# Optimization experiments

Measured on AMD Instinct MI355X. Metric: run time of the kernel, lower is better.

The kernel has to match this reference:

```python
import jax, jax.numpy as jnp
import numpy as np

N = 50000          # nodes
E = 1000000        # edges (k=20 avg degree)
SD = 32            # scalar_dim = hidden_dim//2
VD = 32            # vector_dim = hidden_dim//2
L = 3              # num_layers
SPIN = 2           # spin_symmetry
IN_DIM = 2 * SD + VD + 3   # message MLP input dim = 99
OUT_DIM = SD + VD          # 64


def setup_inputs() -> dict:
    key = jax.random.key(0)
    ks = jax.random.split(key, 12)
    pos = jax.random.uniform(ks[0], (N, 2), dtype=jnp.float32)
    redshift = jax.random.uniform(ks[1], (N, 1), dtype=jnp.float32)
    input_shapes = jax.random.normal(ks[2], (N, 2), dtype=jnp.float32)
    edge_index = jax.random.randint(ks[3], (2, E), 0, N, dtype=jnp.int64)
    # encoder params
    enc_s_w = jax.random.normal(ks[4], (SD, 1), dtype=jnp.float32) * 0.5
    enc_s_b = jax.random.normal(ks[5], (SD,), dtype=jnp.float32) * 0.1
    enc_v_w = jax.random.normal(ks[6], (VD, 2), dtype=jnp.float32) * 0.5
    # per-layer message MLP params, stacked over layers
    W1 = jax.random.normal(ks[7], (L, OUT_DIM, IN_DIM), dtype=jnp.float32) * (1.0 / np.sqrt(IN_DIM))
    b1 = jax.random.normal(ks[8], (L, OUT_DIM), dtype=jnp.float32) * 0.1
    W2 = jax.random.normal(ks[9], (L, OUT_DIM, OUT_DIM), dtype=jnp.float32) * (1.0 / np.sqrt(OUT_DIM))
    b2 = jax.random.normal(ks[10], (L, OUT_DIM), dtype=jnp.float32) * 0.1
    return {"pos": pos, "redshift": redshift, "input_shapes": input_shapes,
            "edge_index": edge_index, "enc_s_w": enc_s_w, "enc_s_b": enc_s_b,
            "enc_v_w": enc_v_w, "W1": W1, "b1": b1, "W2": W2, "b2": b2}


def _frame_layer(h_s, h_v, pos, orientation, src, dst, W1, b1, W2, b2):
    # per-edge geometric features
    dpos = pos[src] - pos[dst]                                   # [E,2]
    dist = jnp.sqrt(jnp.sum(dpos * dpos, axis=1)) + 1e-6          # [E]
    phi_global = jnp.arctan2(dpos[:, 1], dpos[:, 0])              # [E]
    alpha_i = orientation[dst, 0]                                 # [E]
    delta_phi = phi_global - alpha_i
    geo = jnp.stack([dist, jnp.cos(SPIN * delta_phi), jnp.sin(SPIN * delta_phi)], axis=-1)  # [E,3]
    # rotate source vector features into destination local frame
    beta_j = orientation[src, 0]
    rot = (beta_j - alpha_i) * SPIN
    c, s = jnp.cos(rot)[:, None], jnp.sin(rot)[:, None]           # [E,1]
    v_j = h_v[src].reshape(-1, VD // 2, 2)                        # [E,nv,2]
    vx = v_j[..., 0] * c - v_j[..., 1] * s
    vy = v_j[..., 0] * s + v_j[..., 1] * c
    v_rot = jnp.stack([vx, vy], axis=-1).reshape(-1, VD)          # [E,VD]
    # message MLP
    msg_in = jnp.concatenate([h_s[src], h_s[dst], v_rot, geo], axis=-1)  # [E,IN_DIM]
    hid = jax.nn.silu(msg_in @ W1.T + b1)
    raw = hid @ W2.T + b2                                         # [E,OUT_DIM]
    msg_s, msg_v = raw[:, :SD], raw[:, SD:]
    # scatter-add to destination nodes
    out_s = jax.ops.segment_sum(msg_s, dst, num_segments=h_s.shape[0])
    out_v = jax.ops.segment_sum(msg_v, dst, num_segments=h_v.shape[0])
    return h_s + out_s, h_v + out_v


def reference(pos, redshift, input_shapes, edge_index, enc_s_w, enc_s_b, enc_v_w, W1, b1, W2, b2):
    src, dst = edge_index[0], edge_index[1]
    h_s = jax.nn.relu(redshift @ enc_s_w.T + enc_s_b)             # [N,SD]
    h_v = input_shapes @ enc_v_w.T                                # [N,VD]
    orientation = jnp.zeros((pos.shape[0], 1), dtype=pos.dtype)
    for l in range(L):
        h_s, h_v = _frame_layer(h_s, h_v, pos, orientation, src, dst,
                                W1[l], b1[l], W2[l], b2[l])
    return h_s, h_v
```

## Files before the change

### kernel.cpp

```cpp
#include <hip/hip_runtime.h>
#include <hip/hip_bf16.h>

#define WPB 4
#define TILE 16

typedef unsigned short ushort_t;
typedef unsigned int uint_t;

__device__ __forceinline__ float silu_f(float x) {
  return x * __builtin_amdgcn_rcpf(1.0f + __expf(-x));
}
__device__ __forceinline__ int rfl(int x) { return __builtin_amdgcn_readfirstlane(x); }
__device__ __forceinline__ float readlane_f(float v, int l) {
  return __int_as_float(__builtin_amdgcn_readlane(__float_as_int(v), l));
}
__device__ __forceinline__ ushort_t f2bf(float f) {
  uint_t u = __float_as_uint(f);
  u += 0x7FFFu + ((u >> 16) & 1u);
  return (ushort_t)(u >> 16);
}
__device__ __forceinline__ float bf2f(ushort_t b) {
  return __uint_as_float(((uint_t)b) << 16);
}

__global__ void zero_kernel(int* __restrict__ p, int n) {
  int i = blockIdx.x * blockDim.x + threadIdx.x;
  if (i < n) p[i] = 0;
}

__global__ void deg_kernel(const int* __restrict__ ei, int* __restrict__ deg, int E_) {
  int e = blockIdx.x * blockDim.x + threadIdx.x;
  if (e < E_) atomicAdd(&deg[ei[E_ + e]], 1);
}

__global__ __launch_bounds__(1024) void scanA_kernel(const int* __restrict__ deg,
                                                     int* __restrict__ rowptr,
                                                     int* __restrict__ bsum, int n) {
  __shared__ int wsum[16];
  int t = threadIdx.x, lane = t & 63, wid = t >> 6;
  int i = blockIdx.x * 1024 + t;
  int v = (i < n) ? deg[i] : 0;
  int x = v;
#pragma unroll
  for (int off = 1; off < 64; off <<= 1) {
    int y = __shfl_up(x, off);
    if (lane >= off) x += y;
  }
  if (lane == 63) wsum[wid] = x;
  __syncthreads();
  if (t == 0) {
    int run = 0;
#pragma unroll
    for (int w = 0; w < 16; ++w) { int s = wsum[w]; wsum[w] = run; run += s; }
  }
  __syncthreads();
  int inc = x + wsum[wid];
  if (i < n) rowptr[i + 1] = inc;
  if (t == 1023) bsum[blockIdx.x] = inc;
}

__global__ __launch_bounds__(1024) void scanB_kernel(int* __restrict__ bsum, int nb) {
  __shared__ int wsum[16];
  int t = threadIdx.x, lane = t & 63, wid = t >> 6;
  int v = (t < nb) ? bsum[t] : 0;
  int x = v;
#pragma unroll
  for (int off = 1; off < 64; off <<= 1) {
    int y = __shfl_up(x, off);
    if (lane >= off) x += y;
  }
  if (lane == 63) wsum[wid] = x;
  __syncthreads();
  if (t == 0) {
    int run = 0;
#pragma unroll
    for (int w = 0; w < 16; ++w) { int s = wsum[w]; wsum[w] = run; run += s; }
  }
  __syncthreads();
  if (t < nb) bsum[t] = x - v + wsum[wid];
}

__global__ void scanC_kernel(int* __restrict__ rowptr, const int* __restrict__ bsum, int n) {
  int i = blockIdx.x * blockDim.x + threadIdx.x;
  if (i == 0) rowptr[0] = 0;
  if (i < n) rowptr[i + 1] += bsum[i >> 10];
}

__global__ void scatter_kernel(const int* __restrict__ ei, const float* __restrict__ pos,
                               const int* __restrict__ rowptr, int* __restrict__ cursor,
                               float4* __restrict__ edata,
                               int E_, int padE, int N_) {
  int e = blockIdx.x * blockDim.x + threadIdx.x;
  if (e >= padE) return;
  if (e >= E_) {
    edata[e] = make_float4(0.f, 0.f, __int_as_float(0), __int_as_float(N_));
    return;
  }
  int s = ei[e];
  int d = ei[E_ + e];
  int idx = rowptr[d] + atomicAdd(&cursor[d], 1);
  float dx = pos[s * 2 + 0] - pos[d * 2 + 0];
  float dy = pos[s * 2 + 1] - pos[d * 2 + 1];
  float r2 = fmaf(dx, dx, dy * dy);
  float dist = sqrtf(r2) + 1e-6f;
  float c2 = 1.0f, s2 = 0.0f;
  if (r2 > 0.0f) {
    float inv = 1.0f / r2;
    c2 = (dx * dx - dy * dy) * inv;
    s2 = 2.0f * dx * dy * inv;
  }
  uint_t pk = ((uint_t)f2bf(s2) << 16) | (uint_t)f2bf(c2);
  edata[idx] = make_float4(dist, __uint_as_float(pk),
                           __int_as_float(s), __int_as_float(d));
}

__global__ __launch_bounds__(256) void encpsd_kernel(
    const float* __restrict__ redshift, const float* __restrict__ shapes,
    const float* __restrict__ enc_s_w, const float* __restrict__ enc_s_b,
    const float* __restrict__ enc_v_w,
    float* __restrict__ hout, const float* __restrict__ W1l,
    const float* __restrict__ b1l,
    ushort_t* __restrict__ PSh, ushort_t* __restrict__ PDBh,
    float* __restrict__ H, int N_) {
  __shared__ float wsh[99 * 64];
  __shared__ float esw[32], esb[32], evw[64];
  __shared__ __align__(16) float hsh[TILE][64];
  int t = threadIdx.x;
  for (int i = t; i < 99 * 64; i += 256) wsh[i] = W1l[i];
  if (t < 32) { esw[t] = enc_s_w[t]; esb[t] = enc_s_b[t]; }
  else if (t < 96) { evw[t - 32] = enc_v_w[t - 32]; }
  __syncthreads();
  int lane = t & 63, wib = t >> 6;
  float ws_[32], wd_[32], wv_[32];
#pragma unroll
  for (int k = 0; k < 32; ++k) {
    ws_[k] = wsh[lane * 99 + k];
    wd_[k] = wsh[lane * 99 + 32 + k];
    wv_[k] = wsh[lane * 99 + 64 + k];
  }
  float bb1 = b1l[lane];
  const int nTiles = (N_ + TILE - 1) / TILE;
  float* hvbase = hout + (size_t)N_ * 32;
  int tt = t & 127;
  int sn = tt >> 3;
  int sc = tt & 7;
  for (int tile = blockIdx.x; tile < nTiles; tile += gridDim.x) {
    int base = tile * TILE;
    {
      int n = base + sn;
      float4 v = make_float4(0.f, 0.f, 0.f, 0.f);
      if (n < N_) {
        if (t < 128) {
          float r = redshift[n];
#pragma unroll
          for (int jj = 0; jj < 4; ++jj) {
            int j = sc * 4 + jj;
            (&v.x)[jj] = fmaxf(fmaf(r, esw[j], esb[j]), 0.0f);
          }
          *reinterpret_cast<float4*>(hout + (size_t)n * 32 + sc * 4) = v;
        } else {
          float x0 = shapes[n * 2 + 0];
          float x1 = shapes[n * 2 + 1];
#pragma unroll
          for (int jj = 0; jj < 4; ++jj) {
            int j = sc * 4 + jj;
            (&v.x)[jj] = fmaf(x0, evw[j * 2 + 0], x1 * evw[j * 2 + 1]);
          }
          *reinterpret_cast<float4*>(hvbase + (size_t)n * 32 + sc * 4) = v;
        }
      }
      *reinterpret_cast<float4*>(&hsh[sn][(t < 128 ? 0 : 32) + sc * 4]) = v;
    }
    __syncthreads();
#pragma unroll
    for (int q = 0; q < 4; ++q) {
      int r = wib + q * 4;
      int n = base + r;
      if (n < N_) {
        const float4* ha = reinterpret_cast<const float4*>(hsh[r]);
        float ps0 = 0.f, ps1 = 0.f, ps2 = 0.f, ps3 = 0.f, pd0 = 0.f, pd1 = 0.f;
#pragma unroll
        for (int k4 = 0; k4 < 8; ++k4) {
          float4 a = ha[k4];
          float4 v = ha[8 + k4];
          int k = k4 * 4;
          ps0 = fmaf(a.x, ws_[k], ps0);     pd0 = fmaf(a.x, wd_[k], pd0);
          ps1 = fmaf(a.y, ws_[k + 1], ps1); pd1 = fmaf(a.y, wd_[k + 1], pd1);
          ps2 = fmaf(a.z, ws_[k + 2], ps2); pd0 = fmaf(a.z, wd_[k + 2], pd0);
          ps3 = fmaf(a.w, ws_[k + 3], ps3); pd1 = fmaf(a.w, wd_[k + 3], pd1);
          ps0 = fmaf(v.x, wv_[k], ps0);
          ps1 = fmaf(v.y, wv_[k + 1], ps1);
          ps2 = fmaf(v.z, wv_[k + 2], ps2);
          ps3 = fmaf(v.w, wv_[k + 3], ps3);
        }
        PSh[(size_t)n * 64 + lane] = f2bf((ps0 + ps1) + (ps2 + ps3));
        PDBh[(size_t)n * 64 + lane] = f2bf((pd0 + pd1) + bb1);
        H[(size_t)n * 64 + lane] = 0.0f;
      }
    }
    __syncthreads();
  }
}

#define ISSUE(P, G)                                             \
  do {                                                          \
    int t0 = __builtin_amdgcn_readlane(sv, (G) + 0);            \
    int t1 = __builtin_amdgcn_readlane(sv, (G) + 1);            \
    int t2 = __builtin_amdgcn_readlane(sv, (G) + 2);            \
    int t3 = __builtin_amdgcn_readlane(sv, (G) + 3);            \
    int t4 = __builtin_amdgcn_readlane(sv, (G) + 4);            \
    int t5 = __builtin_amdgcn_readlane(sv, (G) + 5);            \
    int t6 = __builtin_amdgcn_readlane(sv, (G) + 6);            \
    int t7 = __builtin_amdgcn_readlane(sv, (G) + 7);            \
    P##0 = PSh[(size_t)t0 * 64 + lane];                         \
    P##1 = PSh[(size_t)t1 * 64 + lane];                         \
    P##2 = PSh[(size_t)t2 * 64 + lane];                         \
    P##3 = PSh[(size_t)t3 * 64 + lane];                         \
    P##4 = PSh[(size_t)t4 * 64 + lane];                         \
    P##5 = PSh[(size_t)t5 * 64 + lane];                         \
    P##6 = PSh[(size_t)t6 * 64 + lane];                         \
    P##7 = PSh[(size_t)t7 * 64 + lane];                         \
  } while (0)

#define FLUSH()                                                          \
  do {                                                                   \
    atomicAdd(H + (size_t)dcur * 64 + lane, acc0 + acc1);                \
    acc0 = acc1 = 0.0f;                                                  \
    dcur = dnext;                                                        \
    pdj = pdj_next;                                                      \
    bmask &= bmask - 1;                                                  \
    bnext = bmask ? (int)__builtin_ctzll(bmask) : 64;                    \
    dnext = (bnext < 64) ? __builtin_amdgcn_readlane(dv, bnext) : dcur;  \
    pdj_next = bf2f(PDBh[(size_t)dnext * 64 + lane]);                    \
  } while (0)

#define EDGE_ONE(PSV, E)                                                     \
  do {                                                                       \
    if ((E) == bnext) FLUSH();                                               \
    float psv = bf2f((ushort_t)(PSV));                                       \
    float di = readlane_f(ed.x, (E));                                        \
    uint_t pk = (uint_t)__builtin_amdgcn_readlane(__float_as_int(ed.y), (E));\
    float c2 = __uint_as_float(pk << 16);                                    \
    float s2 = __uint_as_float(pk & 0xFFFF0000u);                            \
    float pre = fmaf(wg0, di, fmaf(wg1, c2, fmaf(wg2, s2, psv + pdj)));      \
    if ((E) & 1) acc1 += silu_f(pre); else acc0 += silu_f(pre);              \
  } while (0)

#define CONSUME(P, G)                                            \
  do {                                                           \
    EDGE_ONE(P##0, (G) + 0); EDGE_ONE(P##1, (G) + 1);            \
    EDGE_ONE(P##2, (G) + 2); EDGE_ONE(P##3, (G) + 3);            \
    EDGE_ONE(P##4, (G) + 4); EDGE_ONE(P##5, (G) + 5);            \
    EDGE_ONE(P##6, (G) + 6); EDGE_ONE(P##7, (G) + 7);            \
  } while (0)

__global__ __launch_bounds__(256) void edge_kernel(
    const ushort_t* __restrict__ PSh, const ushort_t* __restrict__ PDBh,
    const float4* __restrict__ edata,
    const float* __restrict__ W1l, float* __restrict__ H, int nchunk) {
  int lane = threadIdx.x & 63, wib = threadIdx.x >> 6;
  int chunk = blockIdx.x * WPB + wib;
  if (chunk >= nchunk) return;
  int base = chunk << 6;
  float wg0 = W1l[lane * 99 + 96];
  float wg1 = W1l[lane * 99 + 97];
  float wg2 = W1l[lane * 99 + 98];
  float4 ed = edata[base + lane];
  int sv = __float_as_int(ed.z);
  int dv = __float_as_int(ed.w);
  int dprev = __shfl_up(dv, 1);
  unsigned long long bmask = __ballot(dv != dprev) & ~1ull;
  int dcur = rfl(dv);
  float pdj = bf2f(PDBh[(size_t)dcur * 64 + lane]);
  int bnext = bmask ? (int)__builtin_ctzll(bmask) : 64;
  int dnext = (bnext < 64) ? __builtin_amdgcn_readlane(dv, bnext) : dcur;
  float pdj_next = bf2f(PDBh[(size_t)dnext * 64 + lane]);
  float acc0 = 0.0f, acc1 = 0.0f;
  uint_t pA0, pA1, pA2, pA3, pA4, pA5, pA6, pA7;
  uint_t pB0, pB1, pB2, pB3, pB4, pB5, pB6, pB7;
  uint_t pC0, pC1, pC2, pC3, pC4, pC5, pC6, pC7;
  uint_t pD0, pD1, pD2, pD3, pD4, pD5, pD6, pD7;
  ISSUE(pA, 0);
  ISSUE(pB, 8);
  ISSUE(pC, 16);
  ISSUE(pD, 24);
  CONSUME(pA, 0);
  ISSUE(pA, 32);
  CONSUME(pB, 8);
  ISSUE(pB, 40);
  CONSUME(pC, 16);
  ISSUE(pC, 48);
  CONSUME(pD, 24);
  ISSUE(pD, 56);
  CONSUME(pA, 32);
  CONSUME(pB, 40);
  CONSUME(pC, 48);
  CONSUME(pD, 56);
  atomicAdd(H + (size_t)dcur * 64 + lane, acc0 + acc1);
}

__global__ __launch_bounds__(256) void updproj_kernel(
    float* __restrict__ hout, float* __restrict__ H,
    const int* __restrict__ deg,
    const float* __restrict__ W2l, const float* __restrict__ b2l,
    const float* __restrict__ W1n, const float* __restrict__ b1n,
    ushort_t* __restrict__ PSh, ushort_t* __restrict__ PDBh, int N_) {
  __shared__ float w2sh[64 * 65];
  __shared__ float wsh[99 * 64];
  __shared__ __align__(16) float Hsh[TILE][64];
  int t = threadIdx.x;
  for (int i = t; i < 64 * 64; i += 256) w2sh[(i >> 6) * 65 + (i & 63)] = W2l[i];
  for (int i = t; i < 99 * 64; i += 256) wsh[i] = W1n[i];
  __syncthreads();
  int lane = t & 63, wib = t >> 6;
  float w2[64];
#pragma unroll
  for (int k = 0; k < 64; ++k) w2[k] = w2sh[lane * 65 + k];
  float ws_[32], wd_[32], wv_[32];
#pragma unroll
  for (int k = 0; k < 32; ++k) {
    ws_[k] = wsh[lane * 99 + k];
    wd_[k] = wsh[lane * 99 + 32 + k];
    wv_[k] = wsh[lane * 99 + 64 + k];
  }
  float bb2 = b2l[lane];
  float bb1 = b1n[lane];
  const int nTiles = (N_ + TILE - 1) / TILE;
  size_t plane = (size_t)(lane >> 5) * ((size_t)N_ * 32);
  int sn = t >> 4;
  int sc = t & 15;
  for (int tile = blockIdx.x; tile < nTiles; tile += gridDim.x) {
    int base = tile * TILE;
    {
      int n = base + sn;
      float4 v = (n < N_) ? *reinterpret_cast<const float4*>(H + (size_t)n * 64 + sc * 4)
                          : make_float4(0.f, 0.f, 0.f, 0.f);
      *reinterpret_cast<float4*>(&Hsh[sn][sc * 4]) = v;
    }
    __syncthreads();
#pragma unroll
    for (int q = 0; q < 4; ++q) {
      int r = wib + q * 4;
      int n = base + r;
      if (n < N_) {
        const float4* hm = reinterpret_cast<const float4*>(Hsh[r]);
        float o0 = 0.f, o1 = 0.f;
#pragma unroll
        for (int k4 = 0; k4 < 16; k4 += 2) {
          float4 m0 = hm[k4];
          float4 m1 = hm[k4 + 1];
          o0 = fmaf(m0.x, w2[k4 * 4 + 0], o0);
          o0 = fmaf(m0.y, w2[k4 * 4 + 1], o0);
          o0 = fmaf(m0.z, w2[k4 * 4 + 2], o0);
          o0 = fmaf(m0.w, w2[k4 * 4 + 3], o0);
          o1 = fmaf(m1.x, w2[k4 * 4 + 4], o1);
          o1 = fmaf(m1.y, w2[k4 * 4 + 5], o1);
          o1 = fmaf(m1.z, w2[k4 * 4 + 6], o1);
          o1 = fmaf(m1.w, w2[k4 * 4 + 7], o1);
        }
        float degf = (float)deg[n];
        size_t idx = plane + (size_t)n * 32 + (lane & 31);
        float hnew = hout[idx] + (o0 + o1) + degf * bb2;
        hout[idx] = hnew;
        Hsh[r][lane] = hnew;
        asm volatile("s_waitcnt lgkmcnt(0)" ::: "memory");
        const float4* ha = reinterpret_cast<const float4*>(Hsh[r]);
        float ps0 = 0.f, ps1 = 0.f, ps2 = 0.f, ps3 = 0.f, pd0 = 0.f, pd1 = 0.f;
#pragma unroll
        for (int k4 = 0; k4 < 8; ++k4) {
          float4 a = ha[k4];
          float4 v = ha[8 + k4];
          int k = k4 * 4;
          ps0 = fmaf(a.x, ws_[k], ps0);     pd0 = fmaf(a.x, wd_[k], pd0);
          ps1 = fmaf(a.y, ws_[k + 1], ps1); pd1 = fmaf(a.y, wd_[k + 1], pd1);
          ps2 = fmaf(a.z, ws_[k + 2], ps2); pd0 = fmaf(a.z, wd_[k + 2], pd0);
          ps3 = fmaf(a.w, ws_[k + 3], ps3); pd1 = fmaf(a.w, wd_[k + 3], pd1);
          ps0 = fmaf(v.x, wv_[k], ps0);
          ps1 = fmaf(v.y, wv_[k + 1], ps1);
          ps2 = fmaf(v.z, wv_[k + 2], ps2);
          ps3 = fmaf(v.w, wv_[k + 3], ps3);
        }
        PSh[(size_t)n * 64 + lane] = f2bf((ps0 + ps1) + (ps2 + ps3));
        PDBh[(size_t)n * 64 + lane] = f2bf((pd0 + pd1) + bb1);
        H[(size_t)n * 64 + lane] = 0.0f;
      }
    }
    __syncthreads();
  }
}

__global__ __launch_bounds__(256) void out_kernel(
    float* __restrict__ hout, const float* __restrict__ H,
    const int* __restrict__ deg,
    const float* __restrict__ W2l, const float* __restrict__ b2l, int N_) {
  __shared__ float w2sh[64 * 65];
  __shared__ __align__(16) float Hsh[TILE][64];
  int t = threadIdx.x;
  for (int i = t; i < 64 * 64; i += 256) w2sh[(i >> 6) * 65 + (i & 63)] = W2l[i];
  __syncthreads();
  int lane = t & 63, wib = t >> 6;
  float w2[64];
#pragma unroll
  for (int k = 0; k < 64; ++k) w2[k] = w2sh[lane * 65 + k];
  float bb2 = b2l[lane];
  const int nTiles = (N_ + TILE - 1) / TILE;
  size_t plane = (size_t)(lane >> 5) * ((size_t)N_ * 32);
  int sn = t >> 4;
  int sc = t & 15;
  for (int tile = blockIdx.x; tile < nTiles; tile += gridDim.x) {
    int base = tile * TILE;
    {
      int n = base + sn;
      float4 v = (n < N_) ? *reinterpret_cast<const float4*>(H + (size_t)n * 64 + sc * 4)
                          : make_float4(0.f, 0.f, 0.f, 0.f);
      *reinterpret_cast<float4*>(&Hsh[sn][sc * 4]) = v;
    }
    __syncthreads();
#pragma unroll
    for (int q = 0; q < 4; ++q) {
      int r = wib + q * 4;
      int n = base + r;
      if (n < N_) {
        const float4* hm = reinterpret_cast<const float4*>(Hsh[r]);
        float o0 = 0.f, o1 = 0.f;
#pragma unroll
        for (int k4 = 0; k4 < 16; k4 += 2) {
          float4 m0 = hm[k4];
          float4 m1 = hm[k4 + 1];
          o0 = fmaf(m0.x, w2[k4 * 4 + 0], o0);
          o0 = fmaf(m0.y, w2[k4 * 4 + 1], o0);
          o0 = fmaf(m0.z, w2[k4 * 4 + 2], o0);
          o0 = fmaf(m0.w, w2[k4 * 4 + 3], o0);
          o1 = fmaf(m1.x, w2[k4 * 4 + 4], o1);
          o1 = fmaf(m1.y, w2[k4 * 4 + 5], o1);
          o1 = fmaf(m1.z, w2[k4 * 4 + 6], o1);
          o1 = fmaf(m1.w, w2[k4 * 4 + 7], o1);
        }
        float degf = (float)deg[n];
        size_t idx = plane + (size_t)n * 32 + (lane & 31);
        hout[idx] += (o0 + o1) + degf * bb2;
      }
    }
    __syncthreads();
  }
}

extern "C" void kernel_launch(void* const* d_in, const int* in_sizes, int n_in,
                              void* d_out, int out_size, void* d_ws, size_t ws_size,
                              hipStream_t stream) {
  const float* pos      = (const float*)d_in[0];
  const float* redshift = (const float*)d_in[1];
  const float* shapes   = (const float*)d_in[2];
  const int*   ei       = (const int*)d_in[3];
  const float* enc_s_w  = (const float*)d_in[4];
  const float* enc_s_b  = (const float*)d_in[5];
  const float* enc_v_w  = (const float*)d_in[6];
  const float* W1       = (const float*)d_in[7];
  const float* b1       = (const float*)d_in[8];
  const float* W2       = (const float*)d_in[9];
  const float* b2       = (const float*)d_in[10];

  const int N_ = in_sizes[1];
  const int E_ = in_sizes[3] / 2;
  const int nchunk = (E_ + 63) / 64;
  const int padE = nchunk * 64;

  float4*   edata = (float4*)d_ws;
  float*    H     = (float*)(edata + padE);
  ushort_t* PSh   = (ushort_t*)(H + (size_t)(N_ + 1) * 64);
  ushort_t* PDBh  = PSh + (size_t)N_ * 64;
  int* rowptr = (int*)(PDBh + (size_t)(N_ + 1) * 64);
  int* deg    = rowptr + (N_ + 1);
  int* cursor = deg + N_;
  int* bsum   = cursor + N_;

  float* hout = (float*)d_out;

  zero_kernel<<<dim3((2 * N_ + 255) / 256), dim3(256), 0, stream>>>(deg, 2 * N_);
  deg_kernel<<<dim3((E_ + 255) / 256), dim3(256), 0, stream>>>(ei, deg, E_);
  const int nbA = (N_ + 1023) / 1024;
  scanA_kernel<<<dim3(nbA), dim3(1024), 0, stream>>>(deg, rowptr, bsum, N_);
  scanB_kernel<<<dim3(1), dim3(1024), 0, stream>>>(bsum, nbA);
  scanC_kernel<<<dim3((N_ + 255) / 256), dim3(256), 0, stream>>>(rowptr, bsum, N_);
  scatter_kernel<<<dim3((padE + 255) / 256), dim3(256), 0, stream>>>(
      ei, pos, rowptr, cursor, edata, E_, padE, N_);

  const int edgeBlocks = (nchunk + WPB - 1) / WPB;

  encpsd_kernel<<<dim3(1024), dim3(256), 0, stream>>>(
      redshift, shapes, enc_s_w, enc_s_b, enc_v_w,
      hout, W1, b1, PSh, PDBh, H, N_);

  for (int l = 0; l < 3; ++l) {
    const float* W2l = W2 + (size_t)l * 64 * 64;
    const float* b2l = b2 + (size_t)l * 64;
    edge_kernel<<<dim3(edgeBlocks), dim3(256), 0, stream>>>(
        PSh, PDBh, edata, W1 + (size_t)l * 64 * 99, H, nchunk);
    if (l < 2) {
      updproj_kernel<<<dim3(1024), dim3(256), 0, stream>>>(
          hout, H, deg, W2l, b2l,
          W1 + (size_t)(l + 1) * 64 * 99, b1 + (size_t)(l + 1) * 64,
          PSh, PDBh, N_);
    } else {
      out_kernel<<<dim3(1024), dim3(256), 0, stream>>>(
          hout, H, deg, W2l, b2l, N_);
    }
  }
}
```

Baseline: 321.7 us.

## Bucket destination nodes per block and accumulate edge messages in shared memory

The edge kernel now assigns each block a contiguous range of 64 destination nodes and walks their CSR-sorted edges. Per-destination projections are staged in LDS, and hidden activations are accumulated with LDS atomics, then written to H once per node. This replaces global float atomics and the separate zeroing of H. Padding edges are removed, and a serial tail loop handles leftover edges. Load balance now depends on how edges are spread across node buckets, and the tail path is done by a single wave with unpipelined gathers.

```diff
diff --git a/kernel.cpp b/kernel.cpp
--- a/kernel.cpp
+++ b/kernel.cpp
@@ -3,6 +3,7 @@
 
 #define WPB 4
 #define TILE 16
+#define BNODES 64
 
 typedef unsigned short ushort_t;
 typedef unsigned int uint_t;
@@ -88,14 +89,9 @@
 
 __global__ void scatter_kernel(const int* __restrict__ ei, const float* __restrict__ pos,
                                const int* __restrict__ rowptr, int* __restrict__ cursor,
-                               float4* __restrict__ edata,
-                               int E_, int padE, int N_) {
+                               float4* __restrict__ edata, int E_) {
   int e = blockIdx.x * blockDim.x + threadIdx.x;
-  if (e >= padE) return;
-  if (e >= E_) {
-    edata[e] = make_float4(0.f, 0.f, __int_as_float(0), __int_as_float(N_));
-    return;
-  }
+  if (e >= E_) return;
   int s = ei[e];
   int d = ei[E_ + e];
   int idx = rowptr[d] + atomicAdd(&cursor[d], 1);
@@ -120,8 +116,7 @@
     const float* __restrict__ enc_v_w,
     float* __restrict__ hout, const float* __restrict__ W1l,
     const float* __restrict__ b1l,
-    ushort_t* __restrict__ PSh, ushort_t* __restrict__ PDBh,
-    float* __restrict__ H, int N_) {
+    ushort_t* __restrict__ PSh, ushort_t* __restrict__ PDBh, int N_) {
   __shared__ float wsh[99 * 64];
   __shared__ float esw[32], esb[32], evw[64];
   __shared__ __align__(16) float hsh[TILE][64];
@@ -195,7 +190,6 @@
         }
         PSh[(size_t)n * 64 + lane] = f2bf((ps0 + ps1) + (ps2 + ps3));
         PDBh[(size_t)n * 64 + lane] = f2bf((pd0 + pd1) + bb1);
-        H[(size_t)n * 64 + lane] = 0.0f;
       }
     }
     __syncthreads();
@@ -224,14 +218,14 @@
 
 #define FLUSH()                                                          \
   do {                                                                   \
-    atomicAdd(H + (size_t)dcur * 64 + lane, acc0 + acc1);                \
+    atomicAdd(&Htile[((dcur - nb0) << 6) + lane], acc0 + acc1);          \
     acc0 = acc1 = 0.0f;                                                  \
     dcur = dnext;                                                        \
     pdj = pdj_next;                                                      \
     bmask &= bmask - 1;                                                  \
     bnext = bmask ? (int)__builtin_ctzll(bmask) : 64;                    \
     dnext = (bnext < 64) ? __builtin_amdgcn_readlane(dv, bnext) : dcur;  \
-    pdj_next = bf2f(PDBh[(size_t)dnext * 64 + lane]);                    \
+    pdj_next = bf2f(pdbTile[((dnext - nb0) << 6) + lane]);               \
   } while (0)
 
 #define EDGE_ONE(PSV, E)                                                     \
@@ -256,47 +250,100 @@
 
 __global__ __launch_bounds__(256) void edge_kernel(
     const ushort_t* __restrict__ PSh, const ushort_t* __restrict__ PDBh,
-    const float4* __restrict__ edata,
-    const float* __restrict__ W1l, float* __restrict__ H, int nchunk) {
-  int lane = threadIdx.x & 63, wib = threadIdx.x >> 6;
-  int chunk = blockIdx.x * WPB + wib;
-  if (chunk >= nchunk) return;
-  int base = chunk << 6;
+    const float4* __restrict__ edata, const int* __restrict__ rowptr,
+    const float* __restrict__ W1l, float* __restrict__ H, int N_) {
+  __shared__ float Htile[BNODES * 64];
+  __shared__ ushort_t pdbTile[BNODES * 64];
+  int t = threadIdx.x;
+  int lane = t & 63, wib = t >> 6;
+  int b = blockIdx.x;
+  int nb0 = b << 6;
+  int nrows = min(BNODES, N_ - nb0);
+  for (int i = t; i < BNODES * 16; i += 256)
+    reinterpret_cast<float4*>(Htile)[i] = make_float4(0.f, 0.f, 0.f, 0.f);
+  for (int i = t; i < nrows * 8; i += 256)
+    reinterpret_cast<uint4*>(pdbTile)[i] =
+        reinterpret_cast<const uint4*>(PDBh + (size_t)nb0 * 64)[i];
+  __syncthreads();
+
+  int begin = rfl(rowptr[nb0]);
+  int end = rfl(rowptr[nb0 + nrows]);
+  int cnt = end - begin;
+  int full = cnt >> 6;
+  int tail = cnt & 63;
   float wg0 = W1l[lane * 99 + 96];
   float wg1 = W1l[lane * 99 + 97];
   float wg2 = W1l[lane * 99 + 98];
-  float4 ed = edata[base + lane];
-  int sv = __float_as_int(ed.z);
-  int dv = __float_as_int(ed.w);
-  int dprev = __shfl_up(dv, 1);
-  unsigned long long bmask = __ballot(dv != dprev) & ~1ull;
-  int dcur = rfl(dv);
-  float pdj = bf2f(PDBh[(size_t)dcur * 64 + lane]);
-  int bnext = bmask ? (int)__builtin_ctzll(bmask) : 64;
-  int dnext = (bnext < 64) ? __builtin_amdgcn_readlane(dv, bnext) : dcur;
-  float pdj_next = bf2f(PDBh[(size_t)dnext * 64 + lane]);
-  float acc0 = 0.0f, acc1 = 0.0f;
-  uint_t pA0, pA1, pA2, pA3, pA4, pA5, pA6, pA7;
-  uint_t pB0, pB1, pB2, pB3, pB4, pB5, pB6, pB7;
-  uint_t pC0, pC1, pC2, pC3, pC4, pC5, pC6, pC7;
-  uint_t pD0, pD1, pD2, pD3, pD4, pD5, pD6, pD7;
-  ISSUE(pA, 0);
-  ISSUE(pB, 8);
-  ISSUE(pC, 16);
-  ISSUE(pD, 24);
-  CONSUME(pA, 0);
-  ISSUE(pA, 32);
-  CONSUME(pB, 8);
-  ISSUE(pB, 40);
-  CONSUME(pC, 16);
-  ISSUE(pC, 48);
-  CONSUME(pD, 24);
-  ISSUE(pD, 56);
-  CONSUME(pA, 32);
-  CONSUME(pB, 40);
-  CONSUME(pC, 48);
-  CONSUME(pD, 56);
-  atomicAdd(H + (size_t)dcur * 64 + lane, acc0 + acc1);
+
+  for (int c = wib; c < full; c += WPB) {
+    int cbase = begin + (c << 6);
+    float4 ed = edata[cbase + lane];
+    int sv = __float_as_int(ed.z);
+    int dv = __float_as_int(ed.w);
+    int dprev = __shfl_up(dv, 1);
+    unsigned long long bmask = __ballot(dv != dprev) & ~1ull;
+    int dcur = rfl(dv);
+    float pdj = bf2f(pdbTile[((dcur - nb0) << 6) + lane]);
+    int bnext = bmask ? (int)__builtin_ctzll(bmask) : 64;
+    int dnext = (bnext < 64) ? __builtin_amdgcn_readlane(dv, bnext) : dcur;
+    float pdj_next = bf2f(pdbTile[((dnext - nb0) << 6) + lane]);
+    float acc0 = 0.0f, acc1 = 0.0f;
+    uint_t pA0, pA1, pA2, pA3, pA4, pA5, pA6, pA7;
+    uint_t pB0, pB1, pB2, pB3, pB4, pB5, pB6, pB7;
+    uint_t pC0, pC1, pC2, pC3, pC4, pC5, pC6, pC7;
+    uint_t pD0, pD1, pD2, pD3, pD4, pD5, pD6, pD7;
+    ISSUE(pA, 0);
+    ISSUE(pB, 8);
+    ISSUE(pC, 16);
+    ISSUE(pD, 24);
+    CONSUME(pA, 0);
+    ISSUE(pA, 32);
+    CONSUME(pB, 8);
+    ISSUE(pB, 40);
+    CONSUME(pC, 16);
+    ISSUE(pC, 48);
+    CONSUME(pD, 24);
+    ISSUE(pD, 56);
+    CONSUME(pA, 32);
+    CONSUME(pB, 40);
+    CONSUME(pC, 48);
+    CONSUME(pD, 56);
+    atomicAdd(&Htile[((dcur - nb0) << 6) + lane], acc0 + acc1);
+  }
+
+  if (wib == 0 && tail) {
+    int base2 = begin + (full << 6);
+    float4 ed = (lane < tail) ? edata[base2 + lane]
+                              : make_float4(0.f, 0.f, 0.f, 0.f);
+    int sv = __float_as_int(ed.z);
+    int dv = __float_as_int(ed.w);
+    int dprev = __shfl_up(dv, 1);
+    unsigned long long bmask = __ballot(dv != dprev) & ~1ull;
+    int dcur = rfl(dv);
+    float pdj = bf2f(pdbTile[((dcur - nb0) << 6) + lane]);
+    float acc0 = 0.0f;
+    for (int e = 0; e < tail; ++e) {
+      if ((bmask >> e) & 1ull) {
+        atomicAdd(&Htile[((dcur - nb0) << 6) + lane], acc0);
+        acc0 = 0.0f;
+        dcur = __builtin_amdgcn_readlane(dv, e);
+        pdj = bf2f(pdbTile[((dcur - nb0) << 6) + lane]);
+      }
+      int se = __builtin_amdgcn_readlane(sv, e);
+      float psv = bf2f(PSh[(size_t)se * 64 + lane]);
+      float di = readlane_f(ed.x, e);
+      uint_t pk = (uint_t)__builtin_amdgcn_readlane(__float_as_int(ed.y), e);
+      float c2 = __uint_as_float(pk << 16);
+      float s2 = __uint_as_float(pk & 0xFFFF0000u);
+      float pre = fmaf(wg0, di, fmaf(wg1, c2, fmaf(wg2, s2, psv + pdj)));
+      acc0 += silu_f(pre);
+    }
+    atomicAdd(&Htile[((dcur - nb0) << 6) + lane], acc0);
+  }
+  __syncthreads();
+  float4* dst = reinterpret_cast<float4*>(H + (size_t)nb0 * 64);
+  for (int i = t; i < nrows * 16; i += 256)
+    dst[i] = reinterpret_cast<const float4*>(Htile)[i];
 }
 
 __global__ __launch_bounds__(256) void updproj_kernel(
@@ -382,7 +429,6 @@
         }
         PSh[(size_t)n * 64 + lane] = f2bf((ps0 + ps1) + (ps2 + ps3));
         PDBh[(size_t)n * 64 + lane] = f2bf((pd0 + pd1) + bb1);
-        H[(size_t)n * 64 + lane] = 0.0f;
       }
     }
     __syncthreads();
@@ -462,11 +508,10 @@
 
   const int N_ = in_sizes[1];
   const int E_ = in_sizes[3] / 2;
-  const int nchunk = (E_ + 63) / 64;
-  const int padE = nchunk * 64;
+  const int NBkt = (N_ + BNODES - 1) / BNODES;
 
   float4*   edata = (float4*)d_ws;
-  float*    H     = (float*)(edata + padE);
+  float*    H     = (float*)(edata + E_);
   ushort_t* PSh   = (ushort_t*)(H + (size_t)(N_ + 1) * 64);
   ushort_t* PDBh  = PSh + (size_t)N_ * 64;
   int* rowptr = (int*)(PDBh + (size_t)(N_ + 1) * 64);
@@ -482,20 +527,18 @@
   scanA_kernel<<<dim3(nbA), dim3(1024), 0, stream>>>(deg, rowptr, bsum, N_);
   scanB_kernel<<<dim3(1), dim3(1024), 0, stream>>>(bsum, nbA);
   scanC_kernel<<<dim3((N_ + 255) / 256), dim3(256), 0, stream>>>(rowptr, bsum, N_);
-  scatter_kernel<<<dim3((padE + 255) / 256), dim3(256), 0, stream>>>(
-      ei, pos, rowptr, cursor, edata, E_, padE, N_);
-
-  const int edgeBlocks = (nchunk + WPB - 1) / WPB;
+  scatter_kernel<<<dim3((E_ + 255) / 256), dim3(256), 0, stream>>>(
+      ei, pos, rowptr, cursor, edata, E_);
 
   encpsd_kernel<<<dim3(1024), dim3(256), 0, stream>>>(
       redshift, shapes, enc_s_w, enc_s_b, enc_v_w,
-      hout, W1, b1, PSh, PDBh, H, N_);
+      hout, W1, b1, PSh, PDBh, N_);
 
   for (int l = 0; l < 3; ++l) {
     const float* W2l = W2 + (size_t)l * 64 * 64;
     const float* b2l = b2 + (size_t)l * 64;
-    edge_kernel<<<dim3(edgeBlocks), dim3(256), 0, stream>>>(
-        PSh, PDBh, edata, W1 + (size_t)l * 64 * 99, H, nchunk);
+    edge_kernel<<<dim3(NBkt), dim3(256), 0, stream>>>(
+        PSh, PDBh, edata, rowptr, W1 + (size_t)l * 64 * 99, H, N_);
     if (l < 2) {
       updproj_kernel<<<dim3(1024), dim3(256), 0, stream>>>(
           hout, H, deg, W2l, b2l,
```

New measurement: 408.6 us. 27.0% more time.
